# Kernel tuning notes

Measured on AMD Instinct MI355X. Metric: run time of the kernel, lower is better.

The kernel has to match this reference:

```python
import jax, jax.numpy as jnp
import numpy as np

N, M, C = 32768, 8192, 128
K = 3            # number of interpolation neighbors (PointNet++/RepSurf FP)
EPS_BN = 1e-5    # torch BatchNorm1d default eps
EPS_D = 1e-8     # RepSurf dist_recip eps


def setup_inputs() -> dict:
    key = jax.random.key(0)
    ks = jax.random.split(key, 16)
    s = 0.05
    inp = {
        "pos1": jax.random.normal(ks[0], (N, 3), jnp.float32),
        "pos2": jax.random.normal(ks[1], (M, 3), jnp.float32),
        "feat2": jax.random.normal(ks[2], (M, C), jnp.float32),
    }
    # MLP stack [128,128,128]: Linear + BatchNorm1d (gamma/beta) per layer
    for i in range(3):
        inp[f"W{i}"] = jax.random.normal(ks[3 + i], (C, C), jnp.float32) * s
        inp[f"b{i}"] = jnp.zeros((C,), jnp.float32)
        inp[f"g{i}"] = jnp.ones((C,), jnp.float32)
        inp[f"be{i}"] = jnp.zeros((C,), jnp.float32)
    return inp


def _lin_bn_relu(x, W, b, g, be):
    # Linear -> BatchNorm1d (training-mode batch stats, biased var) -> ReLU
    y = x @ W.T + b
    m = y.mean(axis=0)
    v = y.var(axis=0)
    return jax.nn.relu((y - m) * jax.lax.rsqrt(v + EPS_BN) * g + be)


def reference(pos1, pos2, feat2, W0, b0, g0, be0, W1, b1, g1, be1, W2, b2, g2, be2):
    # squared pairwise distances [N, M] (memory-bound: 1 GB fp32)
    d = ((pos1 ** 2).sum(-1, keepdims=True)
         + (pos2 ** 2).sum(-1)[None, :]
         - 2.0 * (pos1 @ pos2.T))
    neg_d, idx = jax.lax.top_k(-d, K)          # 3 nearest neighbors
    dk = jnp.maximum(-neg_d, 0.0)              # [N, K] squared dists
    w = 1.0 / (dk + EPS_D)
    w = w / w.sum(-1, keepdims=True)           # inverse-distance weights
    # gather neighbor features and interpolate: [N, K, C] -> [N, C]
    interp = jnp.einsum('nkc,nk->nc', feat2[idx], w)
    x = _lin_bn_relu(interp, W0, b0, g0, be0)
    x = _lin_bn_relu(x, W1, b1, g1, be1)
    x = _lin_bn_relu(x, W2, b2, g2, be2)
    return x
```

## Files before the change

kernel.cpp:

```cpp
#include <hip/hip_runtime.h>
#include <math.h>

#define NQ 32768
#define MC 8192
#define CC 128
#define EPS_BN 1e-5f
#define EPS_D  1e-8

#define DBL_BIG 1e300
#define IDX_BIG 0x7fffffff

#define QB  64
#define TB  512
#define NW  8
#define CH  2048
#define HM  (MC / 2)
#define NCH (HM / CH)
#define SLC (CH / NW)
#define KMASK 0xFFFFE000u
#define IMASK 0x1FFFu
#define NSURV 64
#define KNN_B ((NQ / QB) * 2)
#define GEMM_B (NQ / 64)
#define NGRP 8

typedef __attribute__((ext_vector_type(8))) short bf16x8;
typedef __attribute__((ext_vector_type(4))) float floatx4;
typedef unsigned short ushort_t;

__device__ __forceinline__ unsigned umin_(unsigned a, unsigned b) { return a < b ? a : b; }
__device__ __forceinline__ unsigned umax_(unsigned a, unsigned b) { return a > b ? a : b; }

__device__ __forceinline__ unsigned bf16pair(float a, float b) {
    unsigned ua = __float_as_uint(a); ua = (ua + 0x7FFFu + ((ua >> 16) & 1u)) >> 16;
    unsigned ub = __float_as_uint(b); ub = (ub + 0x7FFFu + ((ub >> 16) & 1u)) >> 16;
    return ua | (ub << 16);
}

__global__ __launch_bounds__(TB) void knn_kernel(const float* __restrict__ pos1,
                                                 const float* __restrict__ pos2,
                                                 unsigned* __restrict__ skeys,
                                                 const float* __restrict__ W0,
                                                 const float* __restrict__ W1,
                                                 const float* __restrict__ W2,
                                                 ushort_t* __restrict__ Wbf,
                                                 float* __restrict__ stats) {
    __shared__ __align__(16) float4 sp4[CH * 3 / 4];
    __shared__ unsigned skey[QB][NW * 4];

    if (blockIdx.x >= KNN_B) {
        const int pb = blockIdx.x - KNN_B;
        const int f = pb * TB + threadIdx.x;
        const float* Ws[3] = {W0, W1, W2};
#pragma unroll
        for (int l = 0; l < 3; ++l) {
            const float4 v = ((const float4*)Ws[l])[f];
            unsigned* dst = (unsigned*)(Wbf + (size_t)l * CC * CC);
            dst[f * 2 + 0] = bf16pair(v.x, v.y);
            dst[f * 2 + 1] = bf16pair(v.z, v.w);
        }
        if (pb == 0)
            for (int i = threadIdx.x; i < 3 * NGRP * 256; i += TB) stats[i] = 0.f;
        return;
    }

    const int half = blockIdx.x & 1;
    const int bq   = blockIdx.x >> 1;
    const int wv = threadIdx.x >> 6;
    const int ln = threadIdx.x & 63;
    const int q  = bq * QB + ln;

    const float px = pos1[q * 3 + 0];
    const float py = pos1[q * 3 + 1];
    const float pz = pos1[q * 3 + 2];

    unsigned k0 = 0xFFFFFFFFu, k1 = 0xFFFFFFFFu, k2 = 0xFFFFFFFFu, k3 = 0xFFFFFFFFu;

    for (int c0 = 0; c0 < NCH; ++c0) {
        const int cb = half * HM + c0 * CH;
        __syncthreads();
        {
            const float4* g4 = (const float4*)(pos2 + (size_t)cb * 3);
#pragma unroll
            for (int i = threadIdx.x; i < CH * 3 / 4; i += TB) sp4[i] = g4[i];
        }
        __syncthreads();
        const float4* b4 = sp4 + wv * (SLC * 3 / 4);
        const int jb = cb + wv * SLC;
#pragma unroll 2
        for (int gi = 0; gi < SLC / 4; ++gi) {
            const float4 A = b4[gi * 3 + 0];
            const float4 B = b4[gi * 3 + 1];
            const float4 Cv = b4[gi * 3 + 2];
            const int j = jb + gi * 4;
            const float cx[4] = {A.x, A.w, B.z, Cv.y};
            const float cy[4] = {A.y, B.x, B.w, Cv.z};
            const float cz[4] = {A.z, B.y, Cv.x, Cv.w};
#pragma unroll
            for (int u = 0; u < 4; ++u) {
                const float dx = px - cx[u], dy = py - cy[u], dz = pz - cz[u];
                const float d = fmaf(dx, dx, fmaf(dy, dy, dz * dz));
                unsigned e = (__float_as_uint(d) & KMASK) | (unsigned)(j + u);
                unsigned t;
                t = umin_(k0, e); e = umax_(k0, e); k0 = t;
                t = umin_(k1, e); e = umax_(k1, e); k1 = t;
                t = umin_(k2, e); e = umax_(k2, e); k2 = t;
                k3 = umin_(k3, e);
            }
        }
    }
    skey[ln][wv * 4 + 0] = k0;
    skey[ln][wv * 4 + 1] = k1;
    skey[ln][wv * 4 + 2] = k2;
    skey[ln][wv * 4 + 3] = k3;
    __syncthreads();

#pragma unroll
    for (int t = threadIdx.x * 4; t < threadIdx.x * 4 + 4; ++t) {
        const int ql = t >> 5, slot = t & 31;
        skeys[(size_t)(bq * QB + ql) * NSURV + half * 32 + slot] = skey[ql][slot];
    }
}

template <int MODE>
__global__ __launch_bounds__(256) void gemm_mfma(const float* __restrict__ Xsrc,
                                                 const unsigned* __restrict__ skeys,
                                                 const float* __restrict__ pos1,
                                                 const float* __restrict__ pos2,
                                                 const float* __restrict__ statsIn,
                                                 const float* __restrict__ gIn,
                                                 const float* __restrict__ beIn,
                                                 const ushort_t* __restrict__ Wb,
                                                 const float* __restrict__ bias,
                                                 float* __restrict__ Y,
                                                 float* __restrict__ statsOut) {
    __shared__ __align__(16) short xa[64][136];
    __shared__ __align__(16) short wb[128][136];
    __shared__ float blk_s[CC], blk_q[CC];
    __shared__ float sc_l[CC], sh_l[CC];

    const int row0 = blockIdx.x * 64;

    if constexpr (MODE == 0) {
        __shared__ int   lidx[QB][3];
        __shared__ float lw[QB][3];
        {
            double* rrd = (double*)&xa[0][0];
            int*    rri = (int*)&wb[0][0];
            const int ql = threadIdx.x >> 2;
            const int pp = threadIdx.x & 3;
            const int qg = row0 + ql;
            const double qx = (double)pos1[qg * 3 + 0];
            const double qy = (double)pos1[qg * 3 + 1];
            const double qz = (double)pos1[qg * 3 + 2];
            double b0 = DBL_BIG, b1 = DBL_BIG, b2 = DBL_BIG;
            int    j0 = IDX_BIG, j1 = IDX_BIG, j2 = IDX_BIG;
            const uint4* kp = (const uint4*)(skeys + (size_t)qg * NSURV + pp * 16);
#pragma unroll
            for (int gi = 0; gi < 4; ++gi) {
                const uint4 kk = kp[gi];
                const unsigned ks[4] = {kk.x, kk.y, kk.z, kk.w};
#pragma unroll
                for (int u = 0; u < 4; ++u) {
                    const int id = (int)(ks[u] & IMASK);
                    const double x = (double)pos2[id * 3 + 0];
                    const double y = (double)pos2[id * 3 + 1];
                    const double z = (double)pos2[id * 3 + 2];
                    const double ax = qx - x, ay = qy - y, az = qz - z;
                    const double d = ax * ax + ay * ay + az * az;
                    const bool l2 = (d < b2) || (d == b2 && id < j2);
                    if (l2) {
                        const bool l1 = (d < b1) || (d == b1 && id < j1);
                        const bool l0 = (d < b0) || (d == b0 && id < j0);
                        b2 = l1 ? b1 : d;              j2 = l1 ? j1 : id;
                        b1 = l1 ? (l0 ? b0 : d) : b1;  j1 = l1 ? (l0 ? j0 : id) : j1;
                        b0 = l0 ? d : b0;              j0 = l0 ? id : j0;
                    }
                }
            }
            const int base = (ql * 4 + pp) * 3;
            rrd[base + 0] = b0; rri[base + 0] = j0;
            rrd[base + 1] = b1; rri[base + 1] = j1;
            rrd[base + 2] = b2; rri[base + 2] = j2;
            __syncthreads();
            if (threadIdx.x < QB) {
                const int qq = threadIdx.x;
                double c0 = DBL_BIG, c1 = DBL_BIG, c2 = DBL_BIG;
                int    i0 = IDX_BIG, i1 = IDX_BIG, i2 = IDX_BIG;
#pragma unroll
                for (int s = 0; s < 12; ++s) {
                    const double d = rrd[qq * 12 + s];
                    const int   id = rri[qq * 12 + s];
                    const bool l2 = (d < c2) || (d == c2 && id < i2);
                    if (l2) {
                        const bool l1 = (d < c1) || (d == c1 && id < i1);
                        const bool l0 = (d < c0) || (d == c0 && id < i0);
                        c2 = l1 ? c1 : d;              i2 = l1 ? i1 : id;
                        c1 = l1 ? (l0 ? c0 : d) : c1;  i1 = l1 ? (l0 ? i0 : id) : i1;
                        c0 = l0 ? d : c0;              i0 = l0 ? id : i0;
                    }
                }
                const double r0 = 1.0 / (c0 + EPS_D);
                const double r1 = 1.0 / (c1 + EPS_D);
                const double r2 = 1.0 / (c2 + EPS_D);
                const double inv = 1.0 / (r0 + r1 + r2);
                lidx[qq][0] = i0; lidx[qq][1] = i1; lidx[qq][2] = i2;
                lw[qq][0] = (float)(r0 * inv);
                lw[qq][1] = (float)(r1 * inv);
                lw[qq][2] = (float)(r2 * inv);
            }
            __syncthreads();
        }
        if (threadIdx.x < CC) { blk_s[threadIdx.x] = 0.f; blk_q[threadIdx.x] = 0.f; }
#pragma unroll
        for (int e = threadIdx.x; e < 64 * 32; e += 256) {
            const int r = e >> 5, c4 = e & 31;
            const int i0 = lidx[r][0], i1 = lidx[r][1], i2 = lidx[r][2];
            const float w0 = lw[r][0], w1 = lw[r][1], w2 = lw[r][2];
            const float4 f0 = *(const float4*)&Xsrc[(size_t)i0 * CC + c4 * 4];
            const float4 f1 = *(const float4*)&Xsrc[(size_t)i1 * CC + c4 * 4];
            const float4 f2 = *(const float4*)&Xsrc[(size_t)i2 * CC + c4 * 4];
            float4 v;
            v.x = w0 * f0.x + w1 * f1.x + w2 * f2.x;
            v.y = w0 * f0.y + w1 * f1.y + w2 * f2.y;
            v.z = w0 * f0.z + w1 * f1.z + w2 * f2.z;
            v.w = w0 * f0.w + w1 * f1.w + w2 * f2.w;
            unsigned* dst = (unsigned*)&xa[r][0];
            dst[c4 * 2 + 0] = bf16pair(v.x, v.y);
            dst[c4 * 2 + 1] = bf16pair(v.z, v.w);
        }
    } else {
        if (threadIdx.x < CC) {
            const int c = threadIdx.x;
            float s = 0.f, q = 0.f;
#pragma unroll
            for (int gr = 0; gr < NGRP; ++gr) {
                s += statsIn[gr * 256 + c];
                q += statsIn[gr * 256 + CC + c];
            }
            const float m = s * (1.f / (float)NQ);
            const float v = fmaf(-m, m, q * (1.f / (float)NQ));
            const float rstd = rsqrtf(v + EPS_BN);
            const float scl = gIn[c] * rstd;
            sc_l[c] = scl;
            sh_l[c] = fmaf(-m, scl, beIn[c]);
            blk_s[c] = 0.f; blk_q[c] = 0.f;
        }
        __syncthreads();
#pragma unroll
        for (int e = threadIdx.x; e < 64 * 32; e += 256) {
            const int r = e >> 5, c4 = e & 31;
            const float4 x  = *(const float4*)&Xsrc[(size_t)(row0 + r) * CC + c4 * 4];
            const float4 sc = *(const float4*)&sc_l[c4 * 4];
            const float4 sh = *(const float4*)&sh_l[c4 * 4];
            float4 v;
            v.x = fmaxf(fmaf(x.x, sc.x, sh.x), 0.f);
            v.y = fmaxf(fmaf(x.y, sc.y, sh.y), 0.f);
            v.z = fmaxf(fmaf(x.z, sc.z, sh.z), 0.f);
            v.w = fmaxf(fmaf(x.w, sc.w, sh.w), 0.f);
            unsigned* dst = (unsigned*)&xa[r][0];
            dst[c4 * 2 + 0] = bf16pair(v.x, v.y);
            dst[c4 * 2 + 1] = bf16pair(v.z, v.w);
        }
    }
#pragma unroll
    for (int e = threadIdx.x; e < 128 * 16; e += 256) {
        const int co = e >> 4, seg = e & 15;
        *(float4*)&wb[co][seg * 8] = *(const float4*)&Wb[(size_t)co * CC + seg * 8];
    }
    __syncthreads();

    const int lane = threadIdx.x & 63;
    const int wv = threadIdx.x >> 6;
    const int nn = lane & 15;
    const int quad = lane >> 4;

    floatx4 acc[8] = {};

    const short* arow = &xa[wv * 16 + nn][0];
#pragma unroll
    for (int ks = 0; ks < 4; ++ks) {
        const bf16x8 a = *(const bf16x8*)(arow + ks * 32 + quad * 8);
#pragma unroll
        for (int ct = 0; ct < 8; ++ct) {
            const bf16x8 b = *(const bf16x8*)(&wb[ct * 16 + nn][0] + ks * 32 + quad * 8);
            acc[ct] = __builtin_amdgcn_mfma_f32_16x16x32_bf16(a, b, acc[ct], 0, 0, 0);
        }
    }

#pragma unroll
    for (int ct = 0; ct < 8; ++ct) {
        const float bv = bias[ct * 16 + nn];
        float s = 0.f, qv = 0.f;
#pragma unroll
        for (int r = 0; r < 4; ++r) {
            acc[ct][r] += bv;
            s += acc[ct][r];
            qv = fmaf(acc[ct][r], acc[ct][r], qv);
        }
#pragma unroll
        for (int r = 0; r < 4; ++r)
            Y[(size_t)(row0 + wv * 16 + quad * 4 + r) * CC + ct * 16 + nn] = acc[ct][r];
        s += __shfl_xor(s, 16, 64); s += __shfl_xor(s, 32, 64);
        qv += __shfl_xor(qv, 16, 64); qv += __shfl_xor(qv, 32, 64);
        if (quad == 0) {
            atomicAdd(&blk_s[ct * 16 + nn], s);
            atomicAdd(&blk_q[ct * 16 + nn], qv);
        }
    }
    __syncthreads();
    {
        const int ch = threadIdx.x;
        const float v = (ch < CC) ? blk_s[ch] : blk_q[ch - CC];
        atomicAdd(&statsOut[(blockIdx.x & (NGRP - 1)) * 256 + ch], v);
    }
}

__global__ __launch_bounds__(256) void bn_final(const float* __restrict__ Y,
                                                const float* __restrict__ statsIn,
                                                const float* __restrict__ g,
                                                const float* __restrict__ be,
                                                float* __restrict__ out) {
    __shared__ float sc_l[CC], sh_l[CC];
    if (threadIdx.x < CC) {
        const int c = threadIdx.x;
        float s = 0.f, q = 0.f;
#pragma unroll
        for (int gr = 0; gr < NGRP; ++gr) {
            s += statsIn[gr * 256 + c];
            q += statsIn[gr * 256 + CC + c];
        }
        const float m = s * (1.f / (float)NQ);
        const float v = fmaf(-m, m, q * (1.f / (float)NQ));
        const float rstd = rsqrtf(v + EPS_BN);
        const float scl = g[c] * rstd;
        sc_l[c] = scl;
        sh_l[c] = fmaf(-m, scl, be[c]);
    }
    __syncthreads();
    const float4* Y4 = (const float4*)Y;
    float4* O4 = (float4*)out;
    const int base = blockIdx.x * 2048 + threadIdx.x;
#pragma unroll
    for (int it = 0; it < 8; ++it) {
        const int i4 = base + it * 256;
        const int c4 = (i4 & 31) * 4;
        const float4 y = Y4[i4];
        const float4 s = *(const float4*)&sc_l[c4];
        const float4 h = *(const float4*)&sh_l[c4];
        float4 o;
        o.x = fmaxf(fmaf(y.x, s.x, h.x), 0.f);
        o.y = fmaxf(fmaf(y.y, s.y, h.y), 0.f);
        o.z = fmaxf(fmaf(y.z, s.z, h.z), 0.f);
        o.w = fmaxf(fmaf(y.w, s.w, h.w), 0.f);
        O4[i4] = o;
    }
}

extern "C" void kernel_launch(void* const* d_in, const int* in_sizes, int n_in,
                              void* d_out, int out_size, void* d_ws, size_t ws_size,
                              hipStream_t stream) {
    (void)in_sizes; (void)n_in; (void)out_size; (void)ws_size;

    const float* pos1  = (const float*)d_in[0];
    const float* pos2  = (const float*)d_in[1];
    const float* feat2 = (const float*)d_in[2];
    const float* Wl[3]  = {(const float*)d_in[3], (const float*)d_in[7],  (const float*)d_in[11]};
    const float* bl[3]  = {(const float*)d_in[4], (const float*)d_in[8],  (const float*)d_in[12]};
    const float* gl[3]  = {(const float*)d_in[5], (const float*)d_in[9],  (const float*)d_in[13]};
    const float* bel[3] = {(const float*)d_in[6], (const float*)d_in[10], (const float*)d_in[14]};

    float* ws = (float*)d_ws;
    float* B0   = ws;
    float* B1   = B0 + (size_t)NQ * CC;
    unsigned* skeys = (unsigned*)B1;
    float* stats = B1 + (size_t)NQ * CC;
    ushort_t* Wbf = (ushort_t*)(stats + 3 * NGRP * 256);

    float* st0 = stats + 0 * NGRP * 256;
    float* st1 = stats + 1 * NGRP * 256;
    float* st2 = stats + 2 * NGRP * 256;

    knn_kernel<<<KNN_B + 8, TB, 0, stream>>>(pos1, pos2, skeys,
                                             Wl[0], Wl[1], Wl[2], Wbf, stats);
    gemm_mfma<0><<<GEMM_B, 256, 0, stream>>>(feat2, skeys, pos1, pos2,
                                             nullptr, nullptr, nullptr,
                                             Wbf + 0 * CC * CC, bl[0], B0, st0);
    gemm_mfma<1><<<GEMM_B, 256, 0, stream>>>(B0, nullptr, nullptr, nullptr,
                                             st0, gl[0], bel[0],
                                             Wbf + 1 * CC * CC, bl[1], B1, st1);
    gemm_mfma<1><<<GEMM_B, 256, 0, stream>>>(B1, nullptr, nullptr, nullptr,
                                             st1, gl[1], bel[1],
                                             Wbf + 2 * CC * CC, bl[2], B0, st2);
    bn_final<<<GEMM_B, 256, 0, stream>>>(B0, st2, gl[2], bel[2], (float*)d_out);
}
```

Measured before the change: 217.4 us.

## Store intermediate activations as bf16 and batch top-4 insertion via sorting network

Intermediate GEMM outputs are now written and read as bf16 instead of fp32, halving the bytes moved between the three MLP layers and the final BN pass. The KNN inner loop now sorts four candidates with a small network and merges them with the running top-4 in one bitonic step, replacing four sequential insertions, and raises the unroll factor. The workspace layout is adjusted so skeys no longer aliases B1. Rounding pre-BN activations to bf16 adds some precision loss, while BN statistics are still accumulated in fp32.

Result: faster. 204.6 us (-5.9%).

```diff
diff --git a/kernel.cpp b/kernel.cpp
--- a/kernel.cpp
+++ b/kernel.cpp
@@ -30,12 +30,19 @@
 
 __device__ __forceinline__ unsigned umin_(unsigned a, unsigned b) { return a < b ? a : b; }
 __device__ __forceinline__ unsigned umax_(unsigned a, unsigned b) { return a > b ? a : b; }
+#define KSWAP(a, b) { unsigned t_ = umin_(a, b); b = umax_(a, b); a = t_; }
 
 __device__ __forceinline__ unsigned bf16pair(float a, float b) {
     unsigned ua = __float_as_uint(a); ua = (ua + 0x7FFFu + ((ua >> 16) & 1u)) >> 16;
     unsigned ub = __float_as_uint(b); ub = (ub + 0x7FFFu + ((ub >> 16) & 1u)) >> 16;
     return ua | (ub << 16);
 }
+__device__ __forceinline__ ushort_t bf16one(float a) {
+    unsigned ua = __float_as_uint(a);
+    return (ushort_t)((ua + 0x7FFFu + ((ua >> 16) & 1u)) >> 16);
+}
+__device__ __forceinline__ float bflo(unsigned u) { return __uint_as_float(u << 16); }
+__device__ __forceinline__ float bfhi(unsigned u) { return __uint_as_float(u & 0xFFFF0000u); }
 
 __global__ __launch_bounds__(TB) void knn_kernel(const float* __restrict__ pos1,
                                                  const float* __restrict__ pos2,
@@ -87,7 +94,7 @@
         __syncthreads();
         const float4* b4 = sp4 + wv * (SLC * 3 / 4);
         const int jb = cb + wv * SLC;
-#pragma unroll 2
+#pragma unroll 4
         for (int gi = 0; gi < SLC / 4; ++gi) {
             const float4 A = b4[gi * 3 + 0];
             const float4 B = b4[gi * 3 + 1];
@@ -96,17 +103,22 @@
             const float cx[4] = {A.x, A.w, B.z, Cv.y};
             const float cy[4] = {A.y, B.x, B.w, Cv.z};
             const float cz[4] = {A.z, B.y, Cv.x, Cv.w};
-#pragma unroll
-            for (int u = 0; u < 4; ++u) {
-                const float dx = px - cx[u], dy = py - cy[u], dz = pz - cz[u];
-                const float d = fmaf(dx, dx, fmaf(dy, dy, dz * dz));
-                unsigned e = (__float_as_uint(d) & KMASK) | (unsigned)(j + u);
-                unsigned t;
-                t = umin_(k0, e); e = umax_(k0, e); k0 = t;
-                t = umin_(k1, e); e = umax_(k1, e); k1 = t;
-                t = umin_(k2, e); e = umax_(k2, e); k2 = t;
-                k3 = umin_(k3, e);
+            unsigned e0, e1, e2, e3;
+            {
+                float dx = px - cx[0], dy = py - cy[0], dz = pz - cz[0];
+                e0 = (__float_as_uint(fmaf(dx, dx, fmaf(dy, dy, dz * dz))) & KMASK) | (unsigned)(j + 0);
+                dx = px - cx[1]; dy = py - cy[1]; dz = pz - cz[1];
+                e1 = (__float_as_uint(fmaf(dx, dx, fmaf(dy, dy, dz * dz))) & KMASK) | (unsigned)(j + 1);
+                dx = px - cx[2]; dy = py - cy[2]; dz = pz - cz[2];
+                e2 = (__float_as_uint(fmaf(dx, dx, fmaf(dy, dy, dz * dz))) & KMASK) | (unsigned)(j + 2);
+                dx = px - cx[3]; dy = py - cy[3]; dz = pz - cz[3];
+                e3 = (__float_as_uint(fmaf(dx, dx, fmaf(dy, dy, dz * dz))) & KMASK) | (unsigned)(j + 3);
             }
+            KSWAP(e0, e1); KSWAP(e2, e3); KSWAP(e0, e2); KSWAP(e1, e3); KSWAP(e1, e2);
+            unsigned m0 = umin_(k0, e3), m1 = umin_(k1, e2);
+            unsigned m2 = umin_(k2, e1), m3 = umin_(k3, e0);
+            KSWAP(m0, m2); KSWAP(m1, m3); KSWAP(m0, m1); KSWAP(m2, m3);
+            k0 = m0; k1 = m1; k2 = m2; k3 = m3;
         }
     }
     skey[ln][wv * 4 + 0] = k0;
@@ -123,7 +135,7 @@
 }
 
 template <int MODE>
-__global__ __launch_bounds__(256) void gemm_mfma(const float* __restrict__ Xsrc,
+__global__ __launch_bounds__(256) void gemm_mfma(const void* __restrict__ Xsrc_,
                                                  const unsigned* __restrict__ skeys,
                                                  const float* __restrict__ pos1,
                                                  const float* __restrict__ pos2,
@@ -132,7 +144,7 @@
                                                  const float* __restrict__ beIn,
                                                  const ushort_t* __restrict__ Wb,
                                                  const float* __restrict__ bias,
-                                                 float* __restrict__ Y,
+                                                 ushort_t* __restrict__ Y,
                                                  float* __restrict__ statsOut) {
     __shared__ __align__(16) short xa[64][136];
     __shared__ __align__(16) short wb[128][136];
@@ -142,6 +154,7 @@
     const int row0 = blockIdx.x * 64;
 
     if constexpr (MODE == 0) {
+        const float* feat2 = (const float*)Xsrc_;
         __shared__ int   lidx[QB][3];
         __shared__ float lw[QB][3];
         {
@@ -217,9 +230,9 @@
             const int r = e >> 5, c4 = e & 31;
             const int i0 = lidx[r][0], i1 = lidx[r][1], i2 = lidx[r][2];
             const float w0 = lw[r][0], w1 = lw[r][1], w2 = lw[r][2];
-            const float4 f0 = *(const float4*)&Xsrc[(size_t)i0 * CC + c4 * 4];
-            const float4 f1 = *(const float4*)&Xsrc[(size_t)i1 * CC + c4 * 4];
-            const float4 f2 = *(const float4*)&Xsrc[(size_t)i2 * CC + c4 * 4];
+            const float4 f0 = *(const float4*)&feat2[(size_t)i0 * CC + c4 * 4];
+            const float4 f1 = *(const float4*)&feat2[(size_t)i1 * CC + c4 * 4];
+            const float4 f2 = *(const float4*)&feat2[(size_t)i2 * CC + c4 * 4];
             float4 v;
             v.x = w0 * f0.x + w1 * f1.x + w2 * f2.x;
             v.y = w0 * f0.y + w1 * f1.y + w2 * f2.y;
@@ -230,6 +243,7 @@
             dst[c4 * 2 + 1] = bf16pair(v.z, v.w);
         }
     } else {
+        const ushort_t* Xbf = (const ushort_t*)Xsrc_;
         if (threadIdx.x < CC) {
             const int c = threadIdx.x;
             float s = 0.f, q = 0.f;
@@ -248,19 +262,25 @@
         }
         __syncthreads();
 #pragma unroll
-        for (int e = threadIdx.x; e < 64 * 32; e += 256) {
-            const int r = e >> 5, c4 = e & 31;
-            const float4 x  = *(const float4*)&Xsrc[(size_t)(row0 + r) * CC + c4 * 4];
-            const float4 sc = *(const float4*)&sc_l[c4 * 4];
-            const float4 sh = *(const float4*)&sh_l[c4 * 4];
-            float4 v;
-            v.x = fmaxf(fmaf(x.x, sc.x, sh.x), 0.f);
-            v.y = fmaxf(fmaf(x.y, sc.y, sh.y), 0.f);
-            v.z = fmaxf(fmaf(x.z, sc.z, sh.z), 0.f);
-            v.w = fmaxf(fmaf(x.w, sc.w, sh.w), 0.f);
-            unsigned* dst = (unsigned*)&xa[r][0];
-            dst[c4 * 2 + 0] = bf16pair(v.x, v.y);
-            dst[c4 * 2 + 1] = bf16pair(v.z, v.w);
+        for (int e = threadIdx.x; e < 64 * 16; e += 256) {
+            const int r = e >> 4, c8 = e & 15;
+            const uint4 u = *(const uint4*)&Xbf[(size_t)(row0 + r) * CC + c8 * 8];
+            const float4 s0 = *(const float4*)&sc_l[c8 * 8];
+            const float4 s1 = *(const float4*)&sc_l[c8 * 8 + 4];
+            const float4 h0 = *(const float4*)&sh_l[c8 * 8];
+            const float4 h1 = *(const float4*)&sh_l[c8 * 8 + 4];
+            const float v0 = fmaxf(fmaf(bflo(u.x), s0.x, h0.x), 0.f);
+            const float v1 = fmaxf(fmaf(bfhi(u.x), s0.y, h0.y), 0.f);
+            const float v2 = fmaxf(fmaf(bflo(u.y), s0.z, h0.z), 0.f);
+            const float v3 = fmaxf(fmaf(bfhi(u.y), s0.w, h0.w), 0.f);
+            const float v4 = fmaxf(fmaf(bflo(u.z), s1.x, h1.x), 0.f);
+            const float v5 = fmaxf(fmaf(bfhi(u.z), s1.y, h1.y), 0.f);
+            const float v6 = fmaxf(fmaf(bflo(u.w), s1.z, h1.z), 0.f);
+            const float v7 = fmaxf(fmaf(bfhi(u.w), s1.w, h1.w), 0.f);
+            uint4 o;
+            o.x = bf16pair(v0, v1); o.y = bf16pair(v2, v3);
+            o.z = bf16pair(v4, v5); o.w = bf16pair(v6, v7);
+            *(uint4*)&xa[r][c8 * 8] = o;
         }
     }
 #pragma unroll
@@ -300,7 +320,7 @@
         }
 #pragma unroll
         for (int r = 0; r < 4; ++r)
-            Y[(size_t)(row0 + wv * 16 + quad * 4 + r) * CC + ct * 16 + nn] = acc[ct][r];
+            Y[(size_t)(row0 + wv * 16 + quad * 4 + r) * CC + ct * 16 + nn] = bf16one(acc[ct][r]);
         s += __shfl_xor(s, 16, 64); s += __shfl_xor(s, 32, 64);
         qv += __shfl_xor(qv, 16, 64); qv += __shfl_xor(qv, 32, 64);
         if (quad == 0) {
@@ -316,7 +336,7 @@
     }
 }
 
-__global__ __launch_bounds__(256) void bn_final(const float* __restrict__ Y,
+__global__ __launch_bounds__(256) void bn_final(const ushort_t* __restrict__ Y,
                                                 const float* __restrict__ statsIn,
                                                 const float* __restrict__ g,
                                                 const float* __restrict__ be,
@@ -338,22 +358,27 @@
         sh_l[c] = fmaf(-m, scl, be[c]);
     }
     __syncthreads();
-    const float4* Y4 = (const float4*)Y;
-    float4* O4 = (float4*)out;
-    const int base = blockIdx.x * 2048 + threadIdx.x;
-#pragma unroll
-    for (int it = 0; it < 8; ++it) {
-        const int i4 = base + it * 256;
-        const int c4 = (i4 & 31) * 4;
-        const float4 y = Y4[i4];
-        const float4 s = *(const float4*)&sc_l[c4];
-        const float4 h = *(const float4*)&sh_l[c4];
-        float4 o;
-        o.x = fmaxf(fmaf(y.x, s.x, h.x), 0.f);
-        o.y = fmaxf(fmaf(y.y, s.y, h.y), 0.f);
-        o.z = fmaxf(fmaf(y.z, s.z, h.z), 0.f);
-        o.w = fmaxf(fmaf(y.w, s.w, h.w), 0.f);
-        O4[i4] = o;
+    const int base = blockIdx.x * 1024 + threadIdx.x;
+#pragma unroll
+    for (int it = 0; it < 4; ++it) {
+        const int i8 = base + it * 256;
+        const int c8 = (i8 & 15) * 8;
+        const uint4 u = *(const uint4*)&Y[(size_t)i8 * 8];
+        const float4 s0 = *(const float4*)&sc_l[c8];
+        const float4 s1 = *(const float4*)&sc_l[c8 + 4];
+        const float4 h0 = *(const float4*)&sh_l[c8];
+        const float4 h1 = *(const float4*)&sh_l[c8 + 4];
+        float4 o0, o1;
+        o0.x = fmaxf(fmaf(bflo(u.x), s0.x, h0.x), 0.f);
+        o0.y = fmaxf(fmaf(bfhi(u.x), s0.y, h0.y), 0.f);
+        o0.z = fmaxf(fmaf(bflo(u.y), s0.z, h0.z), 0.f);
+        o0.w = fmaxf(fmaf(bfhi(u.y), s0.w, h0.w), 0.f);
+        o1.x = fmaxf(fmaf(bflo(u.z), s1.x, h1.x), 0.f);
+        o1.y = fmaxf(fmaf(bfhi(u.z), s1.y, h1.y), 0.f);
+        o1.z = fmaxf(fmaf(bflo(u.w), s1.z, h1.z), 0.f);
+        o1.w = fmaxf(fmaf(bfhi(u.w), s1.w, h1.w), 0.f);
+        ((float4*)out)[i8 * 2 + 0] = o0;
+        ((float4*)out)[i8 * 2 + 1] = o1;
     }
 }
 
@@ -371,10 +396,10 @@
     const float* bel[3] = {(const float*)d_in[6], (const float*)d_in[10], (const float*)d_in[14]};
 
     float* ws = (float*)d_ws;
-    float* B0   = ws;
-    float* B1   = B0 + (size_t)NQ * CC;
-    unsigned* skeys = (unsigned*)B1;
-    float* stats = B1 + (size_t)NQ * CC;
+    ushort_t* B0 = (ushort_t*)ws;
+    ushort_t* B1 = B0 + (size_t)NQ * CC;
+    unsigned* skeys = (unsigned*)(B1 + (size_t)NQ * CC);
+    float* stats = (float*)(skeys + (size_t)NQ * NSURV);
     ushort_t* Wbf = (ushort_t*)(stats + 3 * NGRP * 256);
 
     float* st0 = stats + 0 * NGRP * 256;
```
